# Kernel optimization log

Measured on AMD Instinct MI355X. Metric: run time of the kernel, lower is better.

The kernel has to match this reference:

```python
import jax, jax.numpy as jnp
import numpy as np

B, S, D = 4, 2048, 1024
H = 16
DH = D // H  # attention_head_size = 64


def setup_inputs() -> dict:
    key = jax.random.key(0)
    ks = jax.random.split(key, 7)
    scale = 0.02
    return {
        "hidden_states": jax.random.normal(ks[0], (B, S, D), dtype=jnp.float32),
        "Wq": jax.random.normal(ks[1], (D, D), dtype=jnp.float32) * scale,
        "bq": jnp.zeros((D,), dtype=jnp.float32),
        "Wk": jax.random.normal(ks[2], (D, D), dtype=jnp.float32) * scale,
        "bk": jnp.zeros((D,), dtype=jnp.float32),
        "Wv": jax.random.normal(ks[3], (D, D), dtype=jnp.float32) * scale,
        "bv": jnp.zeros((D,), dtype=jnp.float32),
    }


def _split_heads(x):
    # [B, S, D] -> [B, H, S, DH]
    b, s, _ = x.shape
    return x.reshape(b, s, H, DH).transpose(0, 2, 1, 3)


def reference(hidden_states, Wq, bq, Wk, bk, Wv, bv):
    # torch nn.Linear computes x @ W.T + b
    q = _split_heads(hidden_states @ Wq.T + bq)  # [B,H,S,DH]
    k = _split_heads(hidden_states @ Wk.T + bk)
    v = _split_heads(hidden_states @ Wv.T + bv)

    scores = jnp.einsum("bhqd,bhkd->bhqk", q, k) / jnp.sqrt(jnp.float32(DH))
    # original detaches attention probs (LRP-style)
    probs = jax.lax.stop_gradient(jax.nn.softmax(scores, axis=-1))
    ctx = jnp.einsum("bhqk,bhkd->bhqd", probs, v)  # [B,H,S,DH]
    # [B,H,S,DH] -> [B,S,D]
    return ctx.transpose(0, 2, 1, 3).reshape(hidden_states.shape[0], hidden_states.shape[1], D)
```

## Files before the change

kernel.cpp:

```cpp
#include <hip/hip_runtime.h>

typedef _Float16 f16;
typedef f16 f16x2 __attribute__((ext_vector_type(2)));
typedef f16 f16x4 __attribute__((ext_vector_type(4)));
typedef f16 f16x8 __attribute__((ext_vector_type(8)));
typedef float f32x4 __attribute__((ext_vector_type(4)));

#define NB 4
#define NS 2048
#define ND 1024
#define NH 16
#define NDH 64

__device__ __forceinline__ void gl2lds16(const void* g, void* l) {
  __builtin_amdgcn_global_load_lds(
      (const __attribute__((address_space(1))) unsigned int*)g,
      (__attribute__((address_space(3))) unsigned int*)l, 16, 0, 0);
}

__device__ __forceinline__ float fast_exp2(float x) {
  return __builtin_amdgcn_exp2f(x);
}

__device__ __forceinline__ f16x2 pk_f16(float a, float b) {
  return __builtin_bit_cast(f16x2, __builtin_amdgcn_cvt_pkrtz(a, b));
}

__global__ __launch_bounds__(256) void cvt_all(
    const float* __restrict__ X, const float* __restrict__ Wq,
    const float* __restrict__ Wk, const float* __restrict__ Wv,
    f16* __restrict__ Xh, f16* __restrict__ Wh) {
  int b = blockIdx.x;
  const float* src;
  f16* dst;
  int off;
  if (b < 8192)       { src = X;  dst = Xh;               off = 0; }
  else if (b < 9216)  { src = Wq; dst = Wh;               off = 8192; }
  else if (b < 10240) { src = Wk; dst = Wh + (1u << 20);  off = 9216; }
  else                { src = Wv; dst = Wh + (2u << 20);  off = 10240; }
  int i = (b - off) * 256 + threadIdx.x;
  float4 v = ((const float4*)src)[i];
  f16x4 h = {(f16)v.x, (f16)v.y, (f16)v.z, (f16)v.w};
  ((f16x4*)dst)[i] = h;
}

__global__ __launch_bounds__(256) void qkv_gemm(
    const f16* __restrict__ Xh, const f16* __restrict__ Wh,
    const float* __restrict__ bq, const float* __restrict__ bk,
    const float* __restrict__ bv,
    f16* __restrict__ QF, f16* __restrict__ KF, f16* __restrict__ VF) {
  __shared__ f16 Ah[128 * 64];
  __shared__ f16 Bh[128 * 64];
  const int t = threadIdx.x;
  const int tileM = blockIdx.x * 128;
  const int nGlob = blockIdx.y * 128;
  const int mat = nGlob >> 10;
  const int col0 = nGlob & 1023;
  const int wave = t >> 6, lane = t & 63;
  const int mOff = (wave & 1) * 64, nOff = (wave >> 1) * 64;
  const int lr = lane & 15, quad = lane >> 4;

  f32x4 acc[4][4];
#pragma unroll
  for (int i = 0; i < 4; i++)
#pragma unroll
    for (int j = 0; j < 4; j++) acc[i][j] = f32x4{0.f, 0.f, 0.f, 0.f};

  const int srow = t >> 3;
  const int sx = ((t & 7) ^ (srow & 7)) * 8;
  const f16* ag = Xh + (size_t)(tileM + srow) * ND + sx;
  const f16* bg = Wh + (size_t)mat * ND * ND + (size_t)(col0 + srow) * ND + sx;
  const bool qk = (mat < 2);
  const int rx = lr & 7;

  for (int kk = 0; kk < ND; kk += 64) {
    __syncthreads();
    gl2lds16(ag + kk,                       Ah + t * 8);
    gl2lds16(ag + (size_t)32 * ND + kk,     Ah + 2048 + t * 8);
    gl2lds16(ag + (size_t)64 * ND + kk,     Ah + 4096 + t * 8);
    gl2lds16(ag + (size_t)96 * ND + kk,     Ah + 6144 + t * 8);
    gl2lds16(bg + kk,                       Bh + t * 8);
    gl2lds16(bg + (size_t)32 * ND + kk,     Bh + 2048 + t * 8);
    gl2lds16(bg + (size_t)64 * ND + kk,     Bh + 4096 + t * 8);
    gl2lds16(bg + (size_t)96 * ND + kk,     Bh + 6144 + t * 8);
    __syncthreads();
#pragma unroll
    for (int c = 0; c < 2; c++) {
      const int ch = ((c * 4 + quad) ^ rx) * 8;
      f16x8 af[4], bf[4];
#pragma unroll
      for (int i = 0; i < 4; i++)
        af[i] = *(const f16x8*)(Ah + (mOff + i * 16 + lr) * 64 + ch);
#pragma unroll
      for (int j = 0; j < 4; j++)
        bf[j] = *(const f16x8*)(Bh + (nOff + j * 16 + lr) * 64 + ch);
      if (qk) {
#pragma unroll
        for (int i = 0; i < 4; i++)
#pragma unroll
          for (int j = 0; j < 4; j++)
            acc[i][j] = __builtin_amdgcn_mfma_f32_16x16x32_f16(bf[j], af[i], acc[i][j], 0, 0, 0);
      } else {
#pragma unroll
        for (int i = 0; i < 4; i++)
#pragma unroll
          for (int j = 0; j < 4; j++)
            acc[i][j] = __builtin_amdgcn_mfma_f32_16x16x32_f16(af[i], bf[j], acc[i][j], 0, 0, 0);
      }
    }
  }

  if (qk) {
    const float* bias = (mat == 0) ? bq : bk;
    f16* dst = (mat == 0) ? QF : KF;
    const float sc = (mat == 0) ? 0.18033688f : 1.0f;
    const int jstart = (quad & 1) * 4;
#pragma unroll
    for (int j = 0; j < 4; j++) {
      int n0 = col0 + nOff + j * 16;
      int h = n0 >> 6;
      int f = j >> 1;
      int lam = lr + 16 * ((2 * j + (quad >> 1)) & 3);
      float4 bb = *(const float4*)(bias + n0 + quad * 4);
#pragma unroll
      for (int i = 0; i < 4; i++) {
        int sF = tileM + mOff + i * 16;
        int b = sF >> 11, st = (sF & 2047) >> 4;
        int bh = b * NH + h;
        f16x4 v;
#pragma unroll
        for (int r = 0; r < 4; r++) v[r] = (f16)((acc[i][j][r] + (&bb.x)[r]) * sc);
        *(f16x4*)(dst + (((size_t)(bh * 128 + st) * 2 + f) * 64 + lam) * 8 + jstart) = v;
      }
    }
  } else {
#pragma unroll
    for (int j = 0; j < 4; j++) {
      int n = col0 + nOff + j * 16 + lr;
      int h = n >> 6, dt = (n >> 4) & 3;
      float bb = bv[n];
#pragma unroll
      for (int i = 0; i < 4; i++) {
        int sF = tileM + mOff + i * 16;
        int b = sF >> 11;
        int kt2 = (sF & 2047) >> 5;
        int ts = (sF >> 4) & 1;
        int bh = b * NH + h;
        f16x4 v;
#pragma unroll
        for (int r = 0; r < 4; r++) v[r] = (f16)(acc[i][j][r] + bb);
        *(f16x4*)(VF + ((size_t)(bh * 64 + kt2) * 4 + dt) * 512 +
                  (size_t)(quad * 16 + lr) * 8 + 4 * ts) = v;
      }
    }
  }
}

__global__ __launch_bounds__(256, 2) void attn_kernel(
    const f16* __restrict__ QF, const f16* __restrict__ KF,
    const f16* __restrict__ VF, float* __restrict__ out) {
  __shared__ f16 LK[2][2048];
  __shared__ f16 LV[2][2048];
  const int t = threadIdx.x, wave = t >> 6, lane = t & 63;
  const int lr = lane & 15, quad = lane >> 4;
  const int bh = blockIdx.x, qb = blockIdx.y;
  const int bb = bh >> 4, hh = bh & 15;
  const size_t bhOff = (size_t)bh * 131072;
  const f16* Qp = QF + bhOff + (size_t)lane * 8;
  const f16* Kg = KF + bhOff + (size_t)t * 8;
  const f16* Vg = VF + bhOff + (size_t)t * 8;
  const int st0 = qb * 16 + wave * 4;

  f16x8 qf[4][2];
#pragma unroll
  for (int qt = 0; qt < 4; qt++) {
    qf[qt][0] = *(const f16x8*)(Qp + (size_t)(st0 + qt) * 1024);
    qf[qt][1] = *(const f16x8*)(Qp + (size_t)(st0 + qt) * 1024 + 512);
  }

  f32x4 o[4][4];
#pragma unroll
  for (int qt = 0; qt < 4; qt++)
#pragma unroll
    for (int dt = 0; dt < 4; dt++) o[qt][dt] = f32x4{0.f, 0.f, 0.f, 0.f};
  f32x4 lacc[4];
#pragma unroll
  for (int qt = 0; qt < 4; qt++) lacc[qt] = f32x4{0.f, 0.f, 0.f, 0.f};
  const f16x8 ones8 = {(f16)1.f, (f16)1.f, (f16)1.f, (f16)1.f,
                       (f16)1.f, (f16)1.f, (f16)1.f, (f16)1.f};

  gl2lds16(Kg, &LK[0][t * 8]);
  gl2lds16(Vg, &LV[0][t * 8]);
  __syncthreads();

  for (int kt2 = 0; kt2 < 64; ++kt2) {
    const int buf = kt2 & 1;
    const size_t nk = (size_t)((kt2 + 1) & 63) * 2048;
    gl2lds16(Kg + nk, &LK[buf ^ 1][t * 8]);
    gl2lds16(Vg + nk, &LV[buf ^ 1][t * 8]);
    f16x8 kk[4], vv[4];
#pragma unroll
    for (int i = 0; i < 4; i++)
      kk[i] = *(const f16x8*)(&LK[buf][i * 512 + lane * 8]);
#pragma unroll
    for (int i = 0; i < 4; i++)
      vv[i] = *(const f16x8*)(&LV[buf][i * 512 + lane * 8]);
    f32x4 sA[4], sB[4];
#pragma unroll
    for (int qt = 0; qt < 4; qt++) {
      sA[qt] = f32x4{0.f, 0.f, 0.f, 0.f};
      sA[qt] = __builtin_amdgcn_mfma_f32_16x16x32_f16(kk[0], qf[qt][0], sA[qt], 0, 0, 0);
      sA[qt] = __builtin_amdgcn_mfma_f32_16x16x32_f16(kk[1], qf[qt][1], sA[qt], 0, 0, 0);
      sB[qt] = f32x4{0.f, 0.f, 0.f, 0.f};
      sB[qt] = __builtin_amdgcn_mfma_f32_16x16x32_f16(kk[2], qf[qt][0], sB[qt], 0, 0, 0);
      sB[qt] = __builtin_amdgcn_mfma_f32_16x16x32_f16(kk[3], qf[qt][1], sB[qt], 0, 0, 0);
    }
    f16x8 pf[4];
#pragma unroll
    for (int qt = 0; qt < 4; qt++) {
      f16x2 a0 = pk_f16(fast_exp2(sA[qt][0]), fast_exp2(sA[qt][1]));
      f16x2 a1 = pk_f16(fast_exp2(sA[qt][2]), fast_exp2(sA[qt][3]));
      f16x2 b0 = pk_f16(fast_exp2(sB[qt][0]), fast_exp2(sB[qt][1]));
      f16x2 b1 = pk_f16(fast_exp2(sB[qt][2]), fast_exp2(sB[qt][3]));
      f16x4 lo = __builtin_shufflevector(a0, a1, 0, 1, 2, 3);
      f16x4 hi = __builtin_shufflevector(b0, b1, 0, 1, 2, 3);
      pf[qt] = __builtin_shufflevector(lo, hi, 0, 1, 2, 3, 4, 5, 6, 7);
    }
#pragma unroll
    for (int dt = 0; dt < 4; dt++)
#pragma unroll
      for (int qt = 0; qt < 4; qt++)
        o[qt][dt] = __builtin_amdgcn_mfma_f32_16x16x32_f16(pf[qt], vv[dt], o[qt][dt], 0, 0, 0);
#pragma unroll
    for (int qt = 0; qt < 4; qt++)
      lacc[qt] = __builtin_amdgcn_mfma_f32_16x16x32_f16(pf[qt], ones8, lacc[qt], 0, 0, 0);
    __syncthreads();
  }

#pragma unroll
  for (int qt = 0; qt < 4; qt++) {
#pragma unroll
    for (int r = 0; r < 4; r++) {
      float inv = 1.0f / lacc[qt][r];
      int q = qb * 256 + wave * 64 + qt * 16 + quad * 4 + r;
#pragma unroll
      for (int dt = 0; dt < 4; dt++)
        out[((size_t)bb * NS + q) * ND + hh * 64 + dt * 16 + lr] = o[qt][dt][r] * inv;
    }
  }
}

extern "C" void kernel_launch(void* const* d_in, const int* in_sizes, int n_in,
                              void* d_out, int out_size, void* d_ws, size_t ws_size,
                              hipStream_t stream) {
  const float* X  = (const float*)d_in[0];
  const float* Wq = (const float*)d_in[1];
  const float* bq = (const float*)d_in[2];
  const float* Wk = (const float*)d_in[3];
  const float* bk = (const float*)d_in[4];
  const float* Wv = (const float*)d_in[5];
  const float* bv = (const float*)d_in[6];
  float* out = (float*)d_out;

  f16* Xh = (f16*)d_ws;
  f16* Wh = (f16*)((char*)d_ws + (size_t)(16u << 20));
  f16* QF = (f16*)((char*)d_ws + (size_t)(22u << 20));
  f16* KF = (f16*)((char*)d_ws + (size_t)(38u << 20));
  f16* VF = (f16*)((char*)d_ws + (size_t)(54u << 20));

  cvt_all<<<11264, 256, 0, stream>>>(X, Wq, Wk, Wv, Xh, Wh);
  qkv_gemm<<<dim3(64, 24), 256, 0, stream>>>(Xh, Wh, bq, bk, bv, QF, KF, VF);
  attn_kernel<<<dim3(64, 8), 256, 0, stream>>>(QF, KF, VF, out);
}
```

Measured before the change: 217.6 us.

## Software-pipeline attention loop so exp of next tile overlaps PV MFMAs

```diff
diff --git a/kernel.cpp b/kernel.cpp
--- a/kernel.cpp
+++ b/kernel.cpp
@@ -189,22 +189,21 @@
   const f16x8 ones8 = {(f16)1.f, (f16)1.f, (f16)1.f, (f16)1.f,
                        (f16)1.f, (f16)1.f, (f16)1.f, (f16)1.f};
 
+  f16x8 pfP[4], vvP[4];
+
   gl2lds16(Kg, &LK[0][t * 8]);
   gl2lds16(Vg, &LV[0][t * 8]);
   __syncthreads();
-
-  for (int kt2 = 0; kt2 < 64; ++kt2) {
-    const int buf = kt2 & 1;
-    const size_t nk = (size_t)((kt2 + 1) & 63) * 2048;
-    gl2lds16(Kg + nk, &LK[buf ^ 1][t * 8]);
-    gl2lds16(Vg + nk, &LV[buf ^ 1][t * 8]);
-    f16x8 kk[4], vv[4];
+  {
+    f16x8 kk[4];
 #pragma unroll
     for (int i = 0; i < 4; i++)
-      kk[i] = *(const f16x8*)(&LK[buf][i * 512 + lane * 8]);
+      kk[i] = *(const f16x8*)(&LK[0][i * 512 + lane * 8]);
 #pragma unroll
     for (int i = 0; i < 4; i++)
-      vv[i] = *(const f16x8*)(&LV[buf][i * 512 + lane * 8]);
+      vvP[i] = *(const f16x8*)(&LV[0][i * 512 + lane * 8]);
+    gl2lds16(Kg + 2048, &LK[1][t * 8]);
+    gl2lds16(Vg + 2048, &LV[1][t * 8]);
     f32x4 sA[4], sB[4];
 #pragma unroll
     for (int qt = 0; qt < 4; qt++) {
@@ -215,7 +214,6 @@
       sB[qt] = __builtin_amdgcn_mfma_f32_16x16x32_f16(kk[2], qf[qt][0], sB[qt], 0, 0, 0);
       sB[qt] = __builtin_amdgcn_mfma_f32_16x16x32_f16(kk[3], qf[qt][1], sB[qt], 0, 0, 0);
     }
-    f16x8 pf[4];
 #pragma unroll
     for (int qt = 0; qt < 4; qt++) {
       f16x2 a0 = pk_f16(fast_exp2(sA[qt][0]), fast_exp2(sA[qt][1]));
@@ -224,18 +222,66 @@
       f16x2 b1 = pk_f16(fast_exp2(sB[qt][2]), fast_exp2(sB[qt][3]));
       f16x4 lo = __builtin_shufflevector(a0, a1, 0, 1, 2, 3);
       f16x4 hi = __builtin_shufflevector(b0, b1, 0, 1, 2, 3);
-      pf[qt] = __builtin_shufflevector(lo, hi, 0, 1, 2, 3, 4, 5, 6, 7);
+      pfP[qt] = __builtin_shufflevector(lo, hi, 0, 1, 2, 3, 4, 5, 6, 7);
+    }
+  }
+  __syncthreads();
+
+  for (int g = 1; g < 64; ++g) {
+    const int buf = g & 1;
+    f16x8 kk[4], vv[4];
+#pragma unroll
+    for (int i = 0; i < 4; i++)
+      kk[i] = *(const f16x8*)(&LK[buf][i * 512 + lane * 8]);
+#pragma unroll
+    for (int i = 0; i < 4; i++)
+      vv[i] = *(const f16x8*)(&LV[buf][i * 512 + lane * 8]);
+    if (g < 63) {
+      const size_t nk = (size_t)(g + 1) * 2048;
+      gl2lds16(Kg + nk, &LK[buf ^ 1][t * 8]);
+      gl2lds16(Vg + nk, &LV[buf ^ 1][t * 8]);
+    }
+    f32x4 sA[4], sB[4];
+#pragma unroll
+    for (int qt = 0; qt < 4; qt++) {
+      sA[qt] = f32x4{0.f, 0.f, 0.f, 0.f};
+      sA[qt] = __builtin_amdgcn_mfma_f32_16x16x32_f16(kk[0], qf[qt][0], sA[qt], 0, 0, 0);
+      sA[qt] = __builtin_amdgcn_mfma_f32_16x16x32_f16(kk[1], qf[qt][1], sA[qt], 0, 0, 0);
+      sB[qt] = f32x4{0.f, 0.f, 0.f, 0.f};
+      sB[qt] = __builtin_amdgcn_mfma_f32_16x16x32_f16(kk[2], qf[qt][0], sB[qt], 0, 0, 0);
+      sB[qt] = __builtin_amdgcn_mfma_f32_16x16x32_f16(kk[3], qf[qt][1], sB[qt], 0, 0, 0);
     }
 #pragma unroll
     for (int dt = 0; dt < 4; dt++)
 #pragma unroll
       for (int qt = 0; qt < 4; qt++)
-        o[qt][dt] = __builtin_amdgcn_mfma_f32_16x16x32_f16(pf[qt], vv[dt], o[qt][dt], 0, 0, 0);
+        o[qt][dt] = __builtin_amdgcn_mfma_f32_16x16x32_f16(pfP[qt], vvP[dt], o[qt][dt], 0, 0, 0);
 #pragma unroll
     for (int qt = 0; qt < 4; qt++)
-      lacc[qt] = __builtin_amdgcn_mfma_f32_16x16x32_f16(pf[qt], ones8, lacc[qt], 0, 0, 0);
+      lacc[qt] = __builtin_amdgcn_mfma_f32_16x16x32_f16(pfP[qt], ones8, lacc[qt], 0, 0, 0);
+#pragma unroll
+    for (int qt = 0; qt < 4; qt++) {
+      f16x2 a0 = pk_f16(fast_exp2(sA[qt][0]), fast_exp2(sA[qt][1]));
+      f16x2 a1 = pk_f16(fast_exp2(sA[qt][2]), fast_exp2(sA[qt][3]));
+      f16x2 b0 = pk_f16(fast_exp2(sB[qt][0]), fast_exp2(sB[qt][1]));
+      f16x2 b1 = pk_f16(fast_exp2(sB[qt][2]), fast_exp2(sB[qt][3]));
+      f16x4 lo = __builtin_shufflevector(a0, a1, 0, 1, 2, 3);
+      f16x4 hi = __builtin_shufflevector(b0, b1, 0, 1, 2, 3);
+      pfP[qt] = __builtin_shufflevector(lo, hi, 0, 1, 2, 3, 4, 5, 6, 7);
+    }
+#pragma unroll
+    for (int i = 0; i < 4; i++) vvP[i] = vv[i];
     __syncthreads();
   }
+
+#pragma unroll
+  for (int dt = 0; dt < 4; dt++)
+#pragma unroll
+    for (int qt = 0; qt < 4; qt++)
+      o[qt][dt] = __builtin_amdgcn_mfma_f32_16x16x32_f16(pfP[qt], vvP[dt], o[qt][dt], 0, 0, 0);
+#pragma unroll
+  for (int qt = 0; qt < 4; qt++)
+    lacc[qt] = __builtin_amdgcn_mfma_f32_16x16x32_f16(pfP[qt], ones8, lacc[qt], 0, 0, 0);
 
 #pragma unroll
   for (int qt = 0; qt < 4; qt++) {
```

Measured after the change: 216.0 us. Within noise of the previous version (-0.7%).
